# Performance work log

Measured on AMD Instinct MI355X. Metric: run time of the kernel, lower is better.

The kernel has to match this reference:

```python
import jax, jax.numpy as jnp
import numpy as np

H = 64  # hidden_size
I = 8   # input_size
O = 1   # output_size


def setup_inputs() -> dict:
    key = jax.random.key(0)
    ks = jax.random.split(key, 7)
    B, T = 4096, 512
    s_ih = 1.0 / np.sqrt(H)
    inp = {
        "x": jax.random.normal(ks[0], (B, T, I), dtype=jnp.float32),
        # PyTorch LSTM params: W_ih [4H, I], W_hh [4H, H], biases [4H] (gate order i,f,g,o)
        "W_ih": jax.random.uniform(ks[1], (4 * H, I), jnp.float32, -s_ih, s_ih),
        "W_hh": jax.random.uniform(ks[2], (4 * H, H), jnp.float32, -s_ih, s_ih),
        "b_ih": jax.random.uniform(ks[3], (4 * H,), jnp.float32, -s_ih, s_ih),
        "b_hh": jax.random.uniform(ks[4], (4 * H,), jnp.float32, -s_ih, s_ih),
        "W_fc": jax.random.uniform(ks[5], (O, H), jnp.float32, -s_ih, s_ih),
        "b_fc": jax.random.uniform(ks[6], (O,), jnp.float32, -s_ih, s_ih),
    }
    return inp


def _lstm_last_h(x, W_ih, W_hh, b_ih, b_hh):
    B, T, _ = x.shape
    # Precompute input contributions for all timesteps: [T, B, 4H]
    xg = jnp.einsum("bti,gi->tbg", x, W_ih) + (b_ih + b_hh)

    def step(carry, xg_t):
        h, c = carry
        gates = xg_t + h @ W_hh.T  # [B, 4H]
        i, f, g, o = jnp.split(gates, 4, axis=-1)  # torch gate order i,f,g,o
        i = jax.nn.sigmoid(i)
        f = jax.nn.sigmoid(f)
        g = jnp.tanh(g)
        o = jax.nn.sigmoid(o)
        c = f * c + i * g
        h = o * jnp.tanh(c)
        return (h, c), None

    h0 = jnp.zeros((B, H), x.dtype)
    c0 = jnp.zeros((B, H), x.dtype)
    (h_T, _), _ = jax.lax.scan(step, (h0, c0), xg)
    return h_T  # [B, H] == out[:, -1, :]


def reference(x, W_ih, W_hh, b_ih, b_hh, W_fc, b_fc):
    h_T = _lstm_last_h(x, W_ih, W_hh, b_ih, b_hh)
    return h_T @ W_fc.T + b_fc  # [B, O]
```

## Files before the change

### kernel.cpp

```cpp
#include <hip/hip_runtime.h>

#define HSZ 64
#define ISZ 8
#define TSZ 512
#define BTILE 8
#define NW 8
#define KP 104

typedef _Float16 f16;
typedef __attribute__((ext_vector_type(8))) _Float16 f16x8;
typedef __attribute__((ext_vector_type(4))) float f32x4;
typedef unsigned short u16;

__device__ __forceinline__ u16 f16bits(float f) {
    union { f16 h; u16 u; } v; v.h = (f16)f;
    return v.u;
}

__global__ __launch_bounds__(512, 4) void lstm_dual2(
    const float* __restrict__ x,
    const float* __restrict__ W_ih,
    const float* __restrict__ W_hh,
    const float* __restrict__ b_ih,
    const float* __restrict__ b_hh,
    const float* __restrict__ W_fc,
    const float* __restrict__ b_fc,
    float* __restrict__ out)
{
    const int tid = threadIdx.x;
    const int w  = tid >> 6;
    const int l  = tid & 63;
    const int lr = l & 15;
    const int lg = l >> 4;
    const int B0 = blockIdx.x * BTILE;
    const bool lo8 = (lr < 8);

    __shared__ __align__(16) u16 H[2][16][KP];
    __shared__ float red[NW][BTILE];

    for (int i = tid; i < 2 * 16 * KP; i += 512)
        ((u16*)H)[i] = 0;

    const int gate = lr & 3;
    const float sc = (gate == 2) ? -2.885390082f : -1.442695041f;
    f16x8 wa0[2], wa1[2], wa2[2];
    f32x4 bias4[2];
#pragma unroll
    for (int q = 0; q < 2; ++q) {
        const int n  = 2 * w + q;
        const int gc = gate * HSZ + 4 * n + (lr >> 2);
        {
            const float4 a = *reinterpret_cast<const float4*>(&W_hh[gc * HSZ + lg * 8]);
            const float4 b = *reinterpret_cast<const float4*>(&W_hh[gc * HSZ + lg * 8 + 4]);
            wa0[q][0] = (f16)(sc * a.x); wa0[q][1] = (f16)(sc * a.y);
            wa0[q][2] = (f16)(sc * a.z); wa0[q][3] = (f16)(sc * a.w);
            wa0[q][4] = (f16)(sc * b.x); wa0[q][5] = (f16)(sc * b.y);
            wa0[q][6] = (f16)(sc * b.z); wa0[q][7] = (f16)(sc * b.w);
        }
        {
            const float4 a = *reinterpret_cast<const float4*>(&W_hh[gc * HSZ + 32 + lg * 8]);
            const float4 b = *reinterpret_cast<const float4*>(&W_hh[gc * HSZ + 32 + lg * 8 + 4]);
            wa1[q][0] = (f16)(sc * a.x); wa1[q][1] = (f16)(sc * a.y);
            wa1[q][2] = (f16)(sc * a.z); wa1[q][3] = (f16)(sc * a.w);
            wa1[q][4] = (f16)(sc * b.x); wa1[q][5] = (f16)(sc * b.y);
            wa1[q][6] = (f16)(sc * b.z); wa1[q][7] = (f16)(sc * b.w);
        }
#pragma unroll
        for (int j = 0; j < 8; ++j) wa2[q][j] = (f16)0.0f;
        if (lg == 0) {
            const float4 a = *reinterpret_cast<const float4*>(&W_ih[gc * ISZ]);
            const float4 b = *reinterpret_cast<const float4*>(&W_ih[gc * ISZ + 4]);
            wa2[q][0] = (f16)(sc * a.x); wa2[q][1] = (f16)(sc * a.y);
            wa2[q][2] = (f16)(sc * a.z); wa2[q][3] = (f16)(sc * a.w);
            wa2[q][4] = (f16)(sc * b.x); wa2[q][5] = (f16)(sc * b.y);
            wa2[q][6] = (f16)(sc * b.z); wa2[q][7] = (f16)(sc * b.w);
        }
        const int hc = 4 * n + lg;
#pragma unroll
        for (int r = 0; r < 4; ++r) {
            const float s = (r == 2) ? -2.885390082f : -1.442695041f;
            bias4[q][r] = s * (b_ih[r * HSZ + hc] + b_hh[r * HSZ + hc]);
        }
    }

    __syncthreads();

    const float* xptr = x + (size_t)(B0 + (l >> 3)) * TSZ * ISZ + (l & 7);
    if (w == 0)
        H[0][l >> 3][HSZ + (l & 7)] = f16bits(xptr[0]);
    __syncthreads();

    const int hcol = 8 * w + lg + (lo8 ? 0 : 4);
    const int brow = lr & 7;
    const u16* rd0 = &H[0][lr][lg * 8];
    const u16* rd1 = &H[1][lr][lg * 8];
    u16* wrA = &H[0][brow][hcol];
    u16* wrB = &H[1][brow][hcol];
    u16* xsA = &H[0][l >> 3][HSZ + (l & 7)];
    u16* xsB = &H[1][l >> 3][HSZ + (l & 7)];

    float c = 0.0f, h = 0.0f;
    const float L2 = 2.885390082f;

#define STEP(RD, WR, XS, XIDX, XGUARD)                                         \
    {                                                                          \
        float xv = 0.0f;                                                       \
        if ((w == 0) && (XGUARD))                                              \
            xv = xptr[(size_t)(XIDX) * ISZ];                                   \
        const f16x8 b0 = *reinterpret_cast<const f16x8*>(RD);                  \
        const f16x8 b1 = *reinterpret_cast<const f16x8*>(RD + 32);             \
        f16x8 b2 = {};                                                         \
        if (lg == 0)                                                           \
            b2 = *reinterpret_cast<const f16x8*>(RD + 64);                     \
        f32x4 a0 = __builtin_amdgcn_mfma_f32_16x16x32_f16(wa2[0], b2, bias4[0], 0, 0, 0); \
        f32x4 a1 = __builtin_amdgcn_mfma_f32_16x16x32_f16(wa2[1], b2, bias4[1], 0, 0, 0); \
        a0 = __builtin_amdgcn_mfma_f32_16x16x32_f16(wa0[0], b0, a0, 0, 0, 0);  \
        a1 = __builtin_amdgcn_mfma_f32_16x16x32_f16(wa0[1], b0, a1, 0, 0, 0);  \
        a0 = __builtin_amdgcn_mfma_f32_16x16x32_f16(wa1[0], b1, a0, 0, 0, 0);  \
        a1 = __builtin_amdgcn_mfma_f32_16x16x32_f16(wa1[1], b1, a1, 0, 0, 0);  \
        float p0, p1, p2, p3;                                                  \
        {                                                                      \
            const float s0 = __shfl_xor(a1[0], 8);                             \
            const float s1 = __shfl_xor(a1[1], 8);                             \
            const float s2 = __shfl_xor(a1[2], 8);                             \
            const float s3 = __shfl_xor(a1[3], 8);                             \
            p0 = lo8 ? a0[0] : s0;                                             \
            p1 = lo8 ? a0[1] : s1;                                             \
            p2 = lo8 ? a0[2] : s2;                                             \
            p3 = lo8 ? a0[3] : s3;                                             \
        }                                                                      \
        const float ea = __builtin_amdgcn_exp2f(p0);                           \
        const float eb = __builtin_amdgcn_exp2f(p1);                           \
        const float ed = __builtin_amdgcn_exp2f(p2);                           \
        const float es = __builtin_amdgcn_exp2f(p3);                           \
        const float A1 = 1.0f + ea, B1 = 1.0f + eb, D1 = 1.0f + ed;            \
        const float R1 = __builtin_amdgcn_rcpf(A1 * B1 * D1);                  \
        c = fmaf(c * A1, D1, (1.0f - ed) * B1) * R1;                           \
        const float eu = __builtin_amdgcn_exp2f(-L2 * c);                      \
        const float R2 = __builtin_amdgcn_rcpf((1.0f + es) * (1.0f + eu));     \
        h = (1.0f - eu) * R2;                                                  \
        *(WR) = f16bits(h);                                                    \
        if ((w == 0) && (XGUARD))                                              \
            *(XS) = f16bits(xv);                                               \
        __syncthreads();                                                       \
    }

    for (int t = 0; t < TSZ; t += 2) {
        STEP(rd0, wrB, xsB, t + 1, true)
        STEP(rd1, wrA, xsA, t + 2, t < TSZ - 2)
    }
#undef STEP

    float v = h * W_fc[hcol];
    v += __shfl_xor(v, 8);
    v += __shfl_xor(v, 16);
    v += __shfl_xor(v, 32);
    if (l < 8) red[w][l] = v;
    __syncthreads();
    if (tid < BTILE) {
        float s = b_fc[0];
#pragma unroll
        for (int ww = 0; ww < NW; ++ww) s += red[ww][tid];
        out[B0 + tid] = s;
    }
}

extern "C" void kernel_launch(void* const* d_in, const int* in_sizes, int n_in,
                              void* d_out, int out_size, void* d_ws, size_t ws_size,
                              hipStream_t stream) {
    const float* x    = (const float*)d_in[0];
    const float* W_ih = (const float*)d_in[1];
    const float* W_hh = (const float*)d_in[2];
    const float* b_ih = (const float*)d_in[3];
    const float* b_hh = (const float*)d_in[4];
    const float* W_fc = (const float*)d_in[5];
    const float* b_fc = (const float*)d_in[6];
    float* out = (float*)d_out;

    const int B = in_sizes[0] / (TSZ * ISZ);
    lstm_dual2<<<B / BTILE, NW * 64, 0, stream>>>(x, W_ih, W_hh, b_ih, b_hh, W_fc, b_fc, out);
}
```

Baseline: 258.6 us.

## Split block into two wave groups alternating MFMA and activation phases

Doubles the batch tile to 16 rows and the block to 16 waves, split into two groups of 8 that handle 8 batch rows each. While one group runs the MFMA gate matmul for its rows, the other runs the nonlinear activations, so matrix and vector work from independent rows overlap on each step. MFMA sections also raise wave priority via s_setprio. The shared h buffer drops from double-buffered to single-buffered, and there are now two barriers per timestep across 1024 threads, which adds sync cost and limits occupancy.

New measurement: 372.4 us. +44.0%, slower.

```diff
diff --git a/kernel.cpp b/kernel.cpp
--- a/kernel.cpp
+++ b/kernel.cpp
@@ -3,8 +3,8 @@
 #define HSZ 64
 #define ISZ 8
 #define TSZ 512
-#define BTILE 8
-#define NW 8
+#define BTILE 16
+#define NW 16
 #define KP 104
 
 typedef _Float16 f16;
@@ -17,7 +17,7 @@
     return v.u;
 }
 
-__global__ __launch_bounds__(512, 4) void lstm_dual2(
+__global__ __launch_bounds__(1024, 4) void lstm_roles(
     const float* __restrict__ x,
     const float* __restrict__ W_ih,
     const float* __restrict__ W_hh,
@@ -28,17 +28,19 @@
     float* __restrict__ out)
 {
     const int tid = threadIdx.x;
-    const int w  = tid >> 6;
+    const int w   = tid >> 6;
+    const int wg  = w & 7;
+    const int grp = w >> 3;
     const int l  = tid & 63;
     const int lr = l & 15;
     const int lg = l >> 4;
     const int B0 = blockIdx.x * BTILE;
     const bool lo8 = (lr < 8);
 
-    __shared__ __align__(16) u16 H[2][16][KP];
-    __shared__ float red[NW][BTILE];
-
-    for (int i = tid; i < 2 * 16 * KP; i += 512)
+    __shared__ __align__(16) u16 H[BTILE][KP];
+    __shared__ float red[NW][8];
+
+    for (int i = tid; i < BTILE * KP; i += 1024)
         ((u16*)H)[i] = 0;
 
     const int gate = lr & 3;
@@ -47,7 +49,7 @@
     f32x4 bias4[2];
 #pragma unroll
     for (int q = 0; q < 2; ++q) {
-        const int n  = 2 * w + q;
+        const int n  = 2 * wg + q;
         const int gc = gate * HSZ + 4 * n + (lr >> 2);
         {
             const float4 a = *reinterpret_cast<const float4*>(&W_hh[gc * HSZ + lg * 8]);
@@ -85,71 +87,98 @@
 
     __syncthreads();
 
-    const float* xptr = x + (size_t)(B0 + (l >> 3)) * TSZ * ISZ + (l & 7);
-    if (w == 0)
-        H[0][l >> 3][HSZ + (l & 7)] = f16bits(xptr[0]);
+    const float* xptr = x + (size_t)(B0 + grp * 8 + (l >> 3)) * TSZ * ISZ + (l & 7);
+    u16* xsp = &H[grp * 8 + (l >> 3)][HSZ + (l & 7)];
+    if (wg == 0)
+        *xsp = f16bits(xptr[0]);
     __syncthreads();
 
-    const int hcol = 8 * w + lg + (lo8 ? 0 : 4);
-    const int brow = lr & 7;
-    const u16* rd0 = &H[0][lr][lg * 8];
-    const u16* rd1 = &H[1][lr][lg * 8];
-    u16* wrA = &H[0][brow][hcol];
-    u16* wrB = &H[1][brow][hcol];
-    u16* xsA = &H[0][l >> 3][HSZ + (l & 7)];
-    u16* xsB = &H[1][l >> 3][HSZ + (l & 7)];
+    const int brow = grp ? (lr | 8) : (lr & 7);
+    const int hcol = 8 * wg + lg + (lo8 ? 0 : 4);
+    const u16* rdb = &H[lr][lg * 8];
+    u16* wrp = &H[brow][hcol];
 
     float c = 0.0f, h = 0.0f;
+    f32x4 a0, a1;
     const float L2 = 2.885390082f;
 
-#define STEP(RD, WR, XS, XIDX, XGUARD)                                         \
-    {                                                                          \
-        float xv = 0.0f;                                                       \
-        if ((w == 0) && (XGUARD))                                              \
-            xv = xptr[(size_t)(XIDX) * ISZ];                                   \
-        const f16x8 b0 = *reinterpret_cast<const f16x8*>(RD);                  \
-        const f16x8 b1 = *reinterpret_cast<const f16x8*>(RD + 32);             \
-        f16x8 b2 = {};                                                         \
-        if (lg == 0)                                                           \
-            b2 = *reinterpret_cast<const f16x8*>(RD + 64);                     \
-        f32x4 a0 = __builtin_amdgcn_mfma_f32_16x16x32_f16(wa2[0], b2, bias4[0], 0, 0, 0); \
-        f32x4 a1 = __builtin_amdgcn_mfma_f32_16x16x32_f16(wa2[1], b2, bias4[1], 0, 0, 0); \
-        a0 = __builtin_amdgcn_mfma_f32_16x16x32_f16(wa0[0], b0, a0, 0, 0, 0);  \
-        a1 = __builtin_amdgcn_mfma_f32_16x16x32_f16(wa0[1], b0, a1, 0, 0, 0);  \
-        a0 = __builtin_amdgcn_mfma_f32_16x16x32_f16(wa1[0], b1, a0, 0, 0, 0);  \
-        a1 = __builtin_amdgcn_mfma_f32_16x16x32_f16(wa1[1], b1, a1, 0, 0, 0);  \
-        float p0, p1, p2, p3;                                                  \
-        {                                                                      \
-            const float s0 = __shfl_xor(a1[0], 8);                             \
-            const float s1 = __shfl_xor(a1[1], 8);                             \
-            const float s2 = __shfl_xor(a1[2], 8);                             \
-            const float s3 = __shfl_xor(a1[3], 8);                             \
-            p0 = lo8 ? a0[0] : s0;                                             \
-            p1 = lo8 ? a0[1] : s1;                                             \
-            p2 = lo8 ? a0[2] : s2;                                             \
-            p3 = lo8 ? a0[3] : s3;                                             \
-        }                                                                      \
-        const float ea = __builtin_amdgcn_exp2f(p0);                           \
-        const float eb = __builtin_amdgcn_exp2f(p1);                           \
-        const float ed = __builtin_amdgcn_exp2f(p2);                           \
-        const float es = __builtin_amdgcn_exp2f(p3);                           \
-        const float A1 = 1.0f + ea, B1 = 1.0f + eb, D1 = 1.0f + ed;            \
-        const float R1 = __builtin_amdgcn_rcpf(A1 * B1 * D1);                  \
-        c = fmaf(c * A1, D1, (1.0f - ed) * B1) * R1;                           \
-        const float eu = __builtin_amdgcn_exp2f(-L2 * c);                      \
-        const float R2 = __builtin_amdgcn_rcpf((1.0f + es) * (1.0f + eu));     \
-        h = (1.0f - eu) * R2;                                                  \
-        *(WR) = f16bits(h);                                                    \
-        if ((w == 0) && (XGUARD))                                              \
-            *(XS) = f16bits(xv);                                               \
-        __syncthreads();                                                       \
-    }
-
-    for (int t = 0; t < TSZ; t += 2) {
-        STEP(rd0, wrB, xsB, t + 1, true)
-        STEP(rd1, wrA, xsA, t + 2, t < TSZ - 2)
-    }
-#undef STEP
+#define MFMA_BLOCK()                                                            \
+    {                                                                           \
+        const f16x8 b0 = *reinterpret_cast<const f16x8*>(rdb);                  \
+        const f16x8 b1 = *reinterpret_cast<const f16x8*>(rdb + 32);             \
+        f16x8 b2 = {};                                                          \
+        if (lg == 0)                                                            \
+            b2 = *reinterpret_cast<const f16x8*>(rdb + 64);                     \
+        __builtin_amdgcn_s_setprio(1);                                          \
+        a0 = __builtin_amdgcn_mfma_f32_16x16x32_f16(wa2[0], b2, bias4[0], 0, 0, 0); \
+        a1 = __builtin_amdgcn_mfma_f32_16x16x32_f16(wa2[1], b2, bias4[1], 0, 0, 0); \
+        a0 = __builtin_amdgcn_mfma_f32_16x16x32_f16(wa0[0], b0, a0, 0, 0, 0);   \
+        a1 = __builtin_amdgcn_mfma_f32_16x16x32_f16(wa0[1], b0, a1, 0, 0, 0);   \
+        a0 = __builtin_amdgcn_mfma_f32_16x16x32_f16(wa1[0], b1, a0, 0, 0, 0);   \
+        a1 = __builtin_amdgcn_mfma_f32_16x16x32_f16(wa1[1], b1, a1, 0, 0, 0);   \
+        __builtin_amdgcn_s_setprio(0);                                          \
+    }
+
+#define ACT_BLOCK()                                                             \
+    {                                                                           \
+        float p0, p1, p2, p3;                                                   \
+        if (grp == 0) {                                                         \
+            const float s0 = __shfl_xor(a1[0], 8);                              \
+            const float s1 = __shfl_xor(a1[1], 8);                              \
+            const float s2 = __shfl_xor(a1[2], 8);                              \
+            const float s3 = __shfl_xor(a1[3], 8);                              \
+            p0 = lo8 ? a0[0] : s0;  p1 = lo8 ? a0[1] : s1;                      \
+            p2 = lo8 ? a0[2] : s2;  p3 = lo8 ? a0[3] : s3;                      \
+        } else {                                                                \
+            const float s0 = __shfl_xor(a0[0], 8);                              \
+            const float s1 = __shfl_xor(a0[1], 8);                              \
+            const float s2 = __shfl_xor(a0[2], 8);                              \
+            const float s3 = __shfl_xor(a0[3], 8);                              \
+            p0 = lo8 ? s0 : a1[0];  p1 = lo8 ? s1 : a1[1];                      \
+            p2 = lo8 ? s2 : a1[2];  p3 = lo8 ? s3 : a1[3];                      \
+        }                                                                       \
+        const float ea = __builtin_amdgcn_exp2f(p0);                            \
+        const float eb = __builtin_amdgcn_exp2f(p1);                            \
+        const float ed = __builtin_amdgcn_exp2f(p2);                            \
+        const float es = __builtin_amdgcn_exp2f(p3);                            \
+        const float A1 = 1.0f + ea, B1 = 1.0f + eb, D1 = 1.0f + ed;             \
+        const float R1 = __builtin_amdgcn_rcpf(A1 * B1 * D1);                   \
+        c = fmaf(c * A1, D1, (1.0f - ed) * B1) * R1;                            \
+        const float eu = __builtin_amdgcn_exp2f(-L2 * c);                       \
+        const float R2 = __builtin_amdgcn_rcpf((1.0f + es) * (1.0f + eu));      \
+        h = (1.0f - eu) * R2;                                                   \
+        *wrp = f16bits(h);                                                      \
+    }
+
+    for (int t = 0; t < TSZ; ++t) {
+        if (grp == 0) {
+            MFMA_BLOCK()
+        } else {
+            float xv = 0.0f;
+            if (wg == 0 && t > 0)
+                xv = xptr[(size_t)t * ISZ];
+            if (t > 0)
+                ACT_BLOCK()
+            if (wg == 0 && t > 0)
+                *xsp = f16bits(xv);
+        }
+        __syncthreads();
+        if (grp == 1) {
+            MFMA_BLOCK()
+        } else {
+            float xv = 0.0f;
+            if (wg == 0 && t + 1 < TSZ)
+                xv = xptr[(size_t)(t + 1) * ISZ];
+            ACT_BLOCK()
+            if (wg == 0 && t + 1 < TSZ)
+                *xsp = f16bits(xv);
+        }
+        __syncthreads();
+    }
+    if (grp == 1)
+        ACT_BLOCK()
+#undef MFMA_BLOCK
+#undef ACT_BLOCK
 
     float v = h * W_fc[hcol];
     v += __shfl_xor(v, 8);
@@ -159,8 +188,9 @@
     __syncthreads();
     if (tid < BTILE) {
         float s = b_fc[0];
-#pragma unroll
-        for (int ww = 0; ww < NW; ++ww) s += red[ww][tid];
+        const int base = (tid >> 3) * 8;
+#pragma unroll
+        for (int ww = 0; ww < 8; ++ww) s += red[base + ww][tid & 7];
         out[B0 + tid] = s;
     }
 }
@@ -178,5 +208,5 @@
     float* out = (float*)d_out;
 
     const int B = in_sizes[0] / (TSZ * ISZ);
-    lstm_dual2<<<B / BTILE, NW * 64, 0, stream>>>(x, W_ih, W_hh, b_ih, b_hh, W_fc, b_fc, out);
+    lstm_roles<<<B / BTILE, NW * 64, 0, stream>>>(x, W_ih, W_hh, b_ih, b_hh, W_fc, b_fc, out);
 }
```
